# Performance work log

Measured on AMD Instinct MI355X. Metric: run time of the kernel, lower is better.

## Reference

```python
import jax, jax.numpy as jnp
import numpy as np

PRECISION = 127.0

def _quantize(t):
    # PWB physical constraint: clip to [-1,1], then quantize to `precision` levels
    t = jnp.clip(t, -1.0, 1.0)
    return jnp.round(t * PRECISION) / PRECISION

def setup_inputs() -> dict:
    key = jax.random.key(0)
    k1, k2, k3 = jax.random.split(key, 3)
    B, D_in, D_out = 8192, 4096, 4096
    x = jax.random.normal(k1, (B, D_in), dtype=jnp.float32)
    weight = jnp.clip(jax.random.normal(k2, (D_in, D_out), dtype=jnp.float32) * 0.05, -1.0, 1.0)
    bias = jnp.clip(jax.random.normal(k3, (D_out,), dtype=jnp.float32) * 0.05, -1.0, 1.0)
    return {"x": x, "weight": weight, "bias": bias}

def reference(x, weight, bias):
    # Quantized dense: out = relu(x @ Q(W) + Q(b))
    w_q = _quantize(weight)            # [D_in, D_out]
    b_q = _quantize(bias)              # [D_out]
    out = jnp.matmul(x, w_q) + b_q     # [B, D_out]
    return jax.nn.relu(out)
```

## Files before the change

### kernel.cpp

```cpp
#include <hip/hip_runtime.h>
#include <cstdint>
#include <cstddef>


#define MDIM 8192
#define NDIM 4096
#define KDIM 4096
#define XSCALE 20.0f
#define BM 256
#define BN 256
#define BK 64
#define NT (KDIM / BK)

typedef __attribute__((ext_vector_type(4))) int i32x4;
typedef __attribute__((ext_vector_type(16))) int i32x16;
typedef __attribute__((ext_vector_type(16))) char i8x16;

__device__ __forceinline__ int quant_x_i(float v) {
  v = v * XSCALE;
  v = fminf(fmaxf(v, -127.f), 127.f);
  return (int)rintf(v);
}

__device__ __forceinline__ signed char quant_w(float w) {
  w = fminf(fmaxf(w, -1.f), 1.f);
  return (signed char)(int)rintf(w * 127.f);
}

__device__ __forceinline__ int pack4(float4 v) {
  unsigned b0 = (unsigned)quant_x_i(v.x) & 0xFFu;
  unsigned b1 = (unsigned)quant_x_i(v.y) & 0xFFu;
  unsigned b2 = (unsigned)quant_x_i(v.z) & 0xFFu;
  unsigned b3 = (unsigned)quant_x_i(v.w) & 0xFFu;
  return (int)(b0 | (b1 << 8) | (b2 << 16) | (b3 << 24));
}

#define XBLOCKS ((MDIM * (size_t)KDIM) / (256 * 16))
#define WBLOCKS ((KDIM / 64) * (NDIM / 64))

__global__ __launch_bounds__(256) void prep_kernel(const float* __restrict__ x,
                                                   const float* __restrict__ w,
                                                   signed char* __restrict__ xq,
                                                   signed char* __restrict__ wt) {
  __shared__ signed char tile[64][68];
  int bid = blockIdx.x;
  int t = threadIdx.x;
  if (bid < (int)XBLOCKS) {
    const float4* xv = (const float4*)x;
    int* xo = (int*)xq;
#pragma unroll
    for (int j = 0; j < 4; j++) {
      size_t idx = (size_t)bid * 1024 + j * 256 + t;
      float4 v = xv[idx];
      xo[idx] = pack4(v);
    }
  } else {
    int wb = bid - (int)XBLOCKS;
    int n0 = (wb % (NDIM / 64)) * 64;
    int k0 = (wb / (NDIM / 64)) * 64;
    int tr = t >> 4;
    int tc = (t & 15) * 4;
#pragma unroll
    for (int i = 0; i < 4; i++) {
      int r = tr + i * 16;
      float4 v = *(const float4*)(w + (size_t)(k0 + r) * NDIM + n0 + tc);
      tile[r][tc + 0] = quant_w(v.x);
      tile[r][tc + 1] = quant_w(v.y);
      tile[r][tc + 2] = quant_w(v.z);
      tile[r][tc + 3] = quant_w(v.w);
    }
    __syncthreads();
    int nn = t >> 2;
    int kc = (t & 3) * 16;
    i8x16 o;
#pragma unroll
    for (int j = 0; j < 16; j++) o[j] = tile[kc + j][nn];
    *(i8x16*)(wt + (size_t)(n0 + nn) * KDIM + k0 + kc) = o;
  }
}

#define GLDS16(g, l)                                                                   \
  __builtin_amdgcn_global_load_lds((const __attribute__((address_space(1))) void*)(g), \
                                   (__attribute__((address_space(3))) void*)(l), 16, 0, 0)

#define VMW4 asm volatile("s_waitcnt vmcnt(4)" ::: "memory")
#define VMW0 asm volatile("s_waitcnt vmcnt(0)" ::: "memory")
#define VMNONE

#define KSUB(J)                                                                       \
  {                                                                                   \
    i32x4 af[4], bf[2];                                                               \
    _Pragma("unroll") for (int mi = 0; mi < 4; mi++)                                  \
        af[mi] = *(const i32x4*)(rabuf + mi * 32 * BK + coff[J]);                     \
    _Pragma("unroll") for (int ni = 0; ni < 2; ni++)                                  \
        bf[ni] = *(const i32x4*)(rbbuf + ni * 32 * BK + coff[J]);                     \
    __builtin_amdgcn_s_setprio(1);                                                    \
    _Pragma("unroll") for (int mi = 0; mi < 4; mi++)                                  \
        _Pragma("unroll") for (int ni = 0; ni < 2; ni++)                              \
            acc[mi][ni] = __builtin_amdgcn_mfma_i32_32x32x32_i8(                      \
                af[mi], bf[ni], acc[mi][ni], 0, 0, 0);                                \
    __builtin_amdgcn_s_setprio(0);                                                    \
  }

#define KTILE(DO_STAGE, VMWAIT)                                                       \
  {                                                                                   \
    const signed char* rabuf = &lds_a[rb][0] + aoff;                                  \
    const signed char* rbbuf = &lds_b[rb][0] + boff;                                  \
    if (DO_STAGE) {                                                                   \
      signed char* la = &lds_a[sb][0] + w * 1024;                                     \
      signed char* lb = &lds_b[sb][0] + w * 1024;                                     \
      GLDS16(ga, la);                                                                 \
      GLDS16(ga + (size_t)128 * KDIM, la + 8192);                                     \
      GLDS16(gb, lb);                                                                 \
      GLDS16(gb + (size_t)128 * KDIM, lb + 8192);                                     \
      ga += BK;                                                                       \
      gb += BK;                                                                       \
    }                                                                                 \
    KSUB(0)                                                                           \
    KSUB(1)                                                                           \
    VMWAIT;                   \
    __builtin_amdgcn_s_barrier();                                                     \
    rb = (rb + 1 == 3) ? 0 : rb + 1;                                                  \
    sb = (sb + 1 == 3) ? 0 : sb + 1;                                                  \
  }

__global__ __launch_bounds__(512, 2) void gemm_kernel(const signed char* __restrict__ A,
                                                      const signed char* __restrict__ B,
                                                      const float* __restrict__ bias,
                                                      float* __restrict__ C) {
  __shared__ signed char lds_a[3][BM * BK];
  __shared__ signed char lds_b[3][BN * BK];

  const int num_pid_n = NDIM / BN;
  int pid = blockIdx.x;
  pid = (pid & 7) * (512 / 8) + (pid >> 3);
  const int GROUP_M = 8;
  int group_size = GROUP_M * num_pid_n;
  int group_id = pid / group_size;
  int first_m = group_id * GROUP_M;
  int pid_m = first_m + ((pid % group_size) % GROUP_M);
  int pid_n = (pid % group_size) / GROUP_M;

  int t = threadIdx.x;
  int w = t >> 6;
  int lane = t & 63;
  int wm = w >> 2;
  int wn = w & 3;
  int lrow = lane & 31;
  int lk = lane >> 5;

  int scl = (lane & 3) ^ ((lane >> 4) & 3);
  const signed char* ga = A + (size_t)(pid_m * BM + w * 16 + (lane >> 2)) * KDIM + scl * 16;
  const signed char* gb = B + (size_t)(pid_n * BN + w * 16 + (lane >> 2)) * KDIM + scl * 16;

  {
    signed char* la0 = &lds_a[0][0] + w * 1024;
    signed char* lb0 = &lds_b[0][0] + w * 1024;
    signed char* la1 = &lds_a[1][0] + w * 1024;
    signed char* lb1 = &lds_b[1][0] + w * 1024;
    GLDS16(ga, la0);
    GLDS16(ga + (size_t)128 * KDIM, la0 + 8192);
    GLDS16(gb, lb0);
    GLDS16(gb + (size_t)128 * KDIM, lb0 + 8192);
    GLDS16(ga + BK, la1);
    GLDS16(ga + BK + (size_t)128 * KDIM, la1 + 8192);
    GLDS16(gb + BK, lb1);
    GLDS16(gb + BK + (size_t)128 * KDIM, lb1 + 8192);
    ga += 2 * BK;
    gb += 2 * BK;
  }

  const int aoff = (wm * 128 + lrow) * BK;
  const int boff = (wn * 64 + lrow) * BK;
  int swz = (lrow >> 2) & 3;
  int coff[2];
#pragma unroll
  for (int j = 0; j < 2; j++) coff[j] = ((2 * j + lk) ^ swz) * 16;

  i32x16 acc[4][2];
#pragma unroll
  for (int i = 0; i < 4; i++)
#pragma unroll
    for (int j = 0; j < 2; j++)
#pragma unroll
      for (int r = 0; r < 16; r++) acc[i][j][r] = 0;

  VMW4;
  __builtin_amdgcn_s_barrier();

  int rb = 0, sb = 2;
  for (int kt = 0; kt < NT - 2; ++kt) {
    KTILE(1, VMW4);
  }
  KTILE(0, VMW0);
  KTILE(0, VMNONE);
  (void)rb;
  (void)sb;

  const float invs = 1.0f / (127.0f * XSCALE);
  int row_base = pid_m * BM + wm * 128 + 4 * lk;
  int col_base = pid_n * BN + wn * 64 + lrow;
#pragma unroll
  for (int ni = 0; ni < 2; ni++) {
    int col = col_base + ni * 32;
    float b = bias[col];
    b = fminf(fmaxf(b, -1.f), 1.f);
    float bq = rintf(b * 127.f) / 127.f;
#pragma unroll
    for (int mi = 0; mi < 4; mi++) {
      int rbase = row_base + mi * 32;
#pragma unroll
      for (int r = 0; r < 16; r++) {
        int row = rbase + (r & 3) + 8 * (r >> 2);
        float v = (float)acc[mi][ni][r] * invs + bq;
        C[(size_t)row * NDIM + col] = fmaxf(v, 0.f);
      }
    }
  }
}

__global__ __launch_bounds__(256) void fallback_kernel(const float* __restrict__ x,
                                                       const float* __restrict__ w,
                                                       const float* __restrict__ bias,
                                                       float* __restrict__ out) {
  __shared__ float As[16][16];
  __shared__ float Bs[16][17];
  int tx = threadIdx.x & 15, ty = threadIdx.x >> 4;
  int row = blockIdx.y * 16 + ty;
  int col = blockIdx.x * 16 + tx;
  float acc = 0.f;
  for (int k0 = 0; k0 < KDIM; k0 += 16) {
    As[ty][tx] = x[(size_t)row * KDIM + k0 + tx];
    float ww = w[(size_t)(k0 + ty) * NDIM + col];
    ww = fminf(fmaxf(ww, -1.f), 1.f);
    Bs[ty][tx] = rintf(ww * 127.f) / 127.f;
    __syncthreads();
#pragma unroll
    for (int kk = 0; kk < 16; kk++) acc += As[ty][kk] * Bs[kk][tx];
    __syncthreads();
  }
  float b = bias[col];
  b = fminf(fmaxf(b, -1.f), 1.f);
  b = rintf(b * 127.f) / 127.f;
  out[(size_t)row * NDIM + col] = fmaxf(acc + b, 0.f);
}

extern "C" void kernel_launch(void* const* d_in, const int* in_sizes, int n_in,
                              void* d_out, int out_size, void* d_ws, size_t ws_size,
                              hipStream_t stream) {
  const float* x = (const float*)d_in[0];
  const float* wgt = (const float*)d_in[1];
  const float* bias = (const float*)d_in[2];
  float* out = (float*)d_out;

  size_t need = (size_t)MDIM * KDIM + (size_t)KDIM * NDIM;
  if (ws_size < need) {
    dim3 grid(NDIM / 16, MDIM / 16);
    fallback_kernel<<<grid, 256, 0, stream>>>(x, wgt, bias, out);
    return;
  }

  signed char* xq = (signed char*)d_ws;
  signed char* wt = xq + (size_t)MDIM * KDIM;

  prep_kernel<<<(int)(XBLOCKS + WBLOCKS), 256, 0, stream>>>(x, wgt, xq, wt);
  gemm_kernel<<<(MDIM / BM) * (NDIM / BN), 512, 0, stream>>>(xq, wt, bias, out);
}
```

Baseline: 426.8 us.

## Software-pipeline LDS fragment reads with MFMAs using double-buffered register fragments

Splits each K-tile into two halves with separate register fragment sets, so LDS reads for the next sub-step are issued while the current MFMAs run. The first fragment of the next tile is prefetched after the barrier. Global-to-LDS staging is split around the MFMA groups, with extra barriers added to keep the waves in step. This aims to hide LDS read latency behind matrix math, at the cost of more registers and more barriers per tile.

```diff
diff --git a/kernel.cpp b/kernel.cpp
--- a/kernel.cpp
+++ b/kernel.cpp
@@ -87,41 +87,44 @@
 #define VMW0 asm volatile("s_waitcnt vmcnt(0)" ::: "memory")
 #define VMNONE
 
-#define KSUB(J)                                                                       \
+#define READ6(AF, BF, RBUF, J)                                                        \
+  _Pragma("unroll") for (int mi = 0; mi < 4; mi++)                                    \
+      AF[mi] = *(const i32x4*)(&lds_a[RBUF][0] + aoff + mi * 32 * BK + coff[J]);      \
+  _Pragma("unroll") for (int ni = 0; ni < 2; ni++)                                    \
+      BF[ni] = *(const i32x4*)(&lds_b[RBUF][0] + boff + ni * 32 * BK + coff[J]);
+
+#define MFMA8(AF, BF)                                                                 \
+  __builtin_amdgcn_s_setprio(1);                                                      \
+  _Pragma("unroll") for (int mi = 0; mi < 4; mi++)                                    \
+      _Pragma("unroll") for (int ni = 0; ni < 2; ni++)                                \
+          acc[mi][ni] = __builtin_amdgcn_mfma_i32_32x32x32_i8(                        \
+              AF[mi], BF[ni], acc[mi][ni], 0, 0, 0);                                  \
+  __builtin_amdgcn_s_setprio(0);
+
+#define KTILE(DO_STAGE, VMWAIT, DO_NEXT)                                              \
   {                                                                                   \
-    i32x4 af[4], bf[2];                                                               \
-    _Pragma("unroll") for (int mi = 0; mi < 4; mi++)                                  \
-        af[mi] = *(const i32x4*)(rabuf + mi * 32 * BK + coff[J]);                     \
-    _Pragma("unroll") for (int ni = 0; ni < 2; ni++)                                  \
-        bf[ni] = *(const i32x4*)(rbbuf + ni * 32 * BK + coff[J]);                     \
-    __builtin_amdgcn_s_setprio(1);                                                    \
-    _Pragma("unroll") for (int mi = 0; mi < 4; mi++)                                  \
-        _Pragma("unroll") for (int ni = 0; ni < 2; ni++)                              \
-            acc[mi][ni] = __builtin_amdgcn_mfma_i32_32x32x32_i8(                      \
-                af[mi], bf[ni], acc[mi][ni], 0, 0, 0);                                \
-    __builtin_amdgcn_s_setprio(0);                                                    \
-  }
-
-#define KTILE(DO_STAGE, VMWAIT)                                                       \
-  {                                                                                   \
-    const signed char* rabuf = &lds_a[rb][0] + aoff;                                  \
-    const signed char* rbbuf = &lds_b[rb][0] + boff;                                  \
-    if (DO_STAGE) {                                                                   \
+    if (DO_STAGE) {                                   \
       signed char* la = &lds_a[sb][0] + w * 1024;                                     \
-      signed char* lb = &lds_b[sb][0] + w * 1024;                                     \
       GLDS16(ga, la);                                                                 \
       GLDS16(ga + (size_t)128 * KDIM, la + 8192);                                     \
+    }                                                                                 \
+    __builtin_amdgcn_s_barrier();                                           \
+    MFMA8(af0, bf0)                                                                   \
+    READ6(af1, bf1, rb, 1)                                                            \
+    if (DO_STAGE) {                                   \
+      signed char* lb = &lds_b[sb][0] + w * 1024;                                     \
       GLDS16(gb, lb);                                                                 \
       GLDS16(gb + (size_t)128 * KDIM, lb + 8192);                                     \
       ga += BK;                                                                       \
       gb += BK;                                                                       \
     }                                                                                 \
-    KSUB(0)                                                                           \
-    KSUB(1)                                                                           \
-    VMWAIT;                   \
-    __builtin_amdgcn_s_barrier();                                                     \
+    __builtin_amdgcn_s_barrier();                                           \
+    MFMA8(af1, bf1)                                                                   \
+    VMWAIT;         \
+    __builtin_amdgcn_s_barrier();       \
     rb = (rb + 1 == 3) ? 0 : rb + 1;                                                  \
     sb = (sb + 1 == 3) ? 0 : sb + 1;                                                  \
+    if (DO_NEXT) { READ6(af0, bf0, rb, 0) }    \
   }
 
 __global__ __launch_bounds__(512, 2) void gemm_kernel(const signed char* __restrict__ A,
@@ -185,15 +188,18 @@
 #pragma unroll
       for (int r = 0; r < 16; r++) acc[i][j][r] = 0;
 
+  i32x4 af0[4], bf0[2], af1[4], bf1[2];
+
+  int rb = 0, sb = 2;
   VMW4;
   __builtin_amdgcn_s_barrier();
-
-  int rb = 0, sb = 2;
+  READ6(af0, bf0, 0, 0)
+
   for (int kt = 0; kt < NT - 2; ++kt) {
-    KTILE(1, VMW4);
-  }
-  KTILE(0, VMW0);
-  KTILE(0, VMNONE);
+    KTILE(1, VMW4, 1)
+  }
+  KTILE(0, VMW0, 1)
+  KTILE(0, VMNONE, 0)
   (void)rb;
   (void)sb;
 
```

Result: faster. 415.2 us (-2.7%).

## Load A fragments directly to registers from pre-tiled layout, bypassing LDS

Applied to the files above, without the earlier changes.

The prep kernel now writes quantized x in a fragment-ready tiled layout, so the GEMM kernel can load A operands straight from global memory into registers with double-buffered register fragments. LDS staging is kept only for B. This removes A's LDS traffic and LDS footprint, and the wait counts and pipeline are adjusted to match. GROUP_M drops from 8 to 4. The trade-off is more register pressure and exposed global-load latency, since each wave fetches its own A fragments and there is no reuse across waves in the same row.

```diff
diff --git a/kernel.cpp b/kernel.cpp
--- a/kernel.cpp
+++ b/kernel.cpp
@@ -11,6 +11,7 @@
 #define BN 256
 #define BK 64
 #define NT (KDIM / BK)
+#define SLAB 131072
 
 typedef __attribute__((ext_vector_type(4))) int i32x4;
 typedef __attribute__((ext_vector_type(16))) int i32x16;
@@ -48,11 +49,17 @@
   if (bid < (int)XBLOCKS) {
     const float4* xv = (const float4*)x;
     int* xo = (int*)xq;
-#pragma unroll
-    for (int j = 0; j < 4; j++) {
-      size_t idx = (size_t)bid * 1024 + j * 256 + t;
-      float4 v = xv[idx];
-      xo[idx] = pack4(v);
+    int r = bid;
+#pragma unroll
+    for (int jj = 0; jj < 4; jj++) {
+      int q = jj * 256 + t;
+      float4 v = xv[(size_t)r * 1024 + q];
+      int tt = q >> 4;
+      int c = (q >> 2) & 3;
+      int b4 = q & 3;
+      size_t oidx = (size_t)(r >> 5) * 32768 + (size_t)tt * 512 + (size_t)(c >> 1) * 256 +
+                    (size_t)(c & 1) * 128 + (size_t)(r & 31) * 4 + b4;
+      xo[oidx] = pack4(v);
     }
   } else {
     int wb = bid - (int)XBLOCKS;
@@ -83,43 +90,38 @@
   __builtin_amdgcn_global_load_lds((const __attribute__((address_space(1))) void*)(g), \
                                    (__attribute__((address_space(3))) void*)(l), 16, 0, 0)
 
-#define VMW4 asm volatile("s_waitcnt vmcnt(4)" ::: "memory")
+#define VMW10 asm volatile("s_waitcnt vmcnt(10)" ::: "memory")
+#define VMW8 asm volatile("s_waitcnt vmcnt(8)" ::: "memory")
 #define VMW0 asm volatile("s_waitcnt vmcnt(0)" ::: "memory")
-#define VMNONE
-
-#define KSUB(J)                                                                       \
+
+#define ALOAD(AF, GP)                                                                 \
+  _Pragma("unroll") for (int mi = 0; mi < 4; mi++)                                    \
+      _Pragma("unroll") for (int j = 0; j < 2; j++)                                   \
+          AF[mi * 2 + j] = *(const i32x4*)(GP + (size_t)mi * SLAB + j * 1024);        \
+  GP += 2048;
+
+#define KT(AFR, AFN, SB_, SA_, VMWAIT)                                                \
   {                                                                                   \
-    i32x4 af[4], bf[2];                                                               \
-    _Pragma("unroll") for (int mi = 0; mi < 4; mi++)                                  \
-        af[mi] = *(const i32x4*)(rabuf + mi * 32 * BK + coff[J]);                     \
+    i32x4 bfr[4];                                                                     \
     _Pragma("unroll") for (int ni = 0; ni < 2; ni++)                                  \
-        bf[ni] = *(const i32x4*)(rbbuf + ni * 32 * BK + coff[J]);                     \
-    __builtin_amdgcn_s_setprio(1);                                                    \
-    _Pragma("unroll") for (int mi = 0; mi < 4; mi++)                                  \
-        _Pragma("unroll") for (int ni = 0; ni < 2; ni++)                              \
-            acc[mi][ni] = __builtin_amdgcn_mfma_i32_32x32x32_i8(                      \
-                af[mi], bf[ni], acc[mi][ni], 0, 0, 0);                                \
-    __builtin_amdgcn_s_setprio(0);                                                    \
-  }
-
-#define KTILE(DO_STAGE, VMWAIT)                                                       \
-  {                                                                                   \
-    const signed char* rabuf = &lds_a[rb][0] + aoff;                                  \
-    const signed char* rbbuf = &lds_b[rb][0] + boff;                                  \
-    if (DO_STAGE) {                                                                   \
-      signed char* la = &lds_a[sb][0] + w * 1024;                                     \
+        _Pragma("unroll") for (int j = 0; j < 2; j++)                                 \
+            bfr[ni * 2 + j] = *(const i32x4*)(&lds_b[rb][0] + boff + ni * 32 * BK + coff[j]); \
+    if (SB_) {                                                                        \
       signed char* lb = &lds_b[sb][0] + w * 1024;                                     \
-      GLDS16(ga, la);                                                                 \
-      GLDS16(ga + (size_t)128 * KDIM, la + 8192);                                     \
       GLDS16(gb, lb);                                                                 \
       GLDS16(gb + (size_t)128 * KDIM, lb + 8192);                                     \
-      ga += BK;                                                                       \
       gb += BK;                                                                       \
     }                                                                                 \
-    KSUB(0)                                                                           \
-    KSUB(1)                                                                           \
-    VMWAIT;                   \
-    __builtin_amdgcn_s_barrier();                                                     \
+    if (SA_) { ALOAD(AFN, gaf) }                                                      \
+    VMWAIT;                    \
+    __builtin_amdgcn_s_setprio(1);                                                    \
+    _Pragma("unroll") for (int j = 0; j < 2; j++)                                     \
+        _Pragma("unroll") for (int mi = 0; mi < 4; mi++)                              \
+            _Pragma("unroll") for (int ni = 0; ni < 2; ni++)                          \
+                acc[mi][ni] = __builtin_amdgcn_mfma_i32_32x32x32_i8(                  \
+                    AFR[mi * 2 + j], bfr[ni * 2 + j], acc[mi][ni], 0, 0, 0);          \
+    __builtin_amdgcn_s_setprio(0);                                                    \
+    __builtin_amdgcn_s_barrier();      \
     rb = (rb + 1 == 3) ? 0 : rb + 1;                                                  \
     sb = (sb + 1 == 3) ? 0 : sb + 1;                                                  \
   }
@@ -128,13 +130,12 @@
                                                       const signed char* __restrict__ B,
                                                       const float* __restrict__ bias,
                                                       float* __restrict__ C) {
-  __shared__ signed char lds_a[3][BM * BK];
   __shared__ signed char lds_b[3][BN * BK];
 
   const int num_pid_n = NDIM / BN;
   int pid = blockIdx.x;
   pid = (pid & 7) * (512 / 8) + (pid >> 3);
-  const int GROUP_M = 8;
+  const int GROUP_M = 4;
   int group_size = GROUP_M * num_pid_n;
   int group_id = pid / group_size;
   int first_m = group_id * GROUP_M;
@@ -150,27 +151,10 @@
   int lk = lane >> 5;
 
   int scl = (lane & 3) ^ ((lane >> 4) & 3);
-  const signed char* ga = A + (size_t)(pid_m * BM + w * 16 + (lane >> 2)) * KDIM + scl * 16;
   const signed char* gb = B + (size_t)(pid_n * BN + w * 16 + (lane >> 2)) * KDIM + scl * 16;
 
-  {
-    signed char* la0 = &lds_a[0][0] + w * 1024;
-    signed char* lb0 = &lds_b[0][0] + w * 1024;
-    signed char* la1 = &lds_a[1][0] + w * 1024;
-    signed char* lb1 = &lds_b[1][0] + w * 1024;
-    GLDS16(ga, la0);
-    GLDS16(ga + (size_t)128 * KDIM, la0 + 8192);
-    GLDS16(gb, lb0);
-    GLDS16(gb + (size_t)128 * KDIM, lb0 + 8192);
-    GLDS16(ga + BK, la1);
-    GLDS16(ga + BK + (size_t)128 * KDIM, la1 + 8192);
-    GLDS16(gb + BK, lb1);
-    GLDS16(gb + BK + (size_t)128 * KDIM, lb1 + 8192);
-    ga += 2 * BK;
-    gb += 2 * BK;
-  }
-
-  const int aoff = (wm * 128 + lrow) * BK;
+  const signed char* gaf = A + (size_t)(pid_m * 8 + wm * 4) * SLAB + lane * 16;
+
   const int boff = (wn * 64 + lrow) * BK;
   int swz = (lrow >> 2) & 3;
   int coff[2];
@@ -185,15 +169,28 @@
 #pragma unroll
       for (int r = 0; r < 16; r++) acc[i][j][r] = 0;
 
-  VMW4;
+  i32x4 afA[8], afB[8];
+
+  {
+    signed char* lb0 = &lds_b[0][0] + w * 1024;
+    signed char* lb1 = &lds_b[1][0] + w * 1024;
+    GLDS16(gb, lb0);
+    GLDS16(gb + (size_t)128 * KDIM, lb0 + 8192);
+    GLDS16(gb + BK, lb1);
+    GLDS16(gb + BK + (size_t)128 * KDIM, lb1 + 8192);
+    gb += 2 * BK;
+  }
+  ALOAD(afA, gaf)
+  VMW8;
   __builtin_amdgcn_s_barrier();
 
   int rb = 0, sb = 2;
-  for (int kt = 0; kt < NT - 2; ++kt) {
-    KTILE(1, VMW4);
-  }
-  KTILE(0, VMW0);
-  KTILE(0, VMNONE);
+  for (int kt = 0; kt < 31; ++kt) {
+    KT(afA, afB, 1, 1, VMW10)
+    KT(afB, afA, 1, 1, VMW10)
+  }
+  KT(afA, afB, 0, 1, VMW8)
+  KT(afB, afA, 0, 0, VMW0)
   (void)rb;
   (void)sb;
 
```

Result: slower. 444.1 us (+4.1%).
